# Kernel tuning notes

Hardware: AMD Instinct MI355X
Metric: run time of the kernel (lower is better)

Reference implementation:

```python
import jax, jax.numpy as jnp
import numpy as np

PI = float(np.pi)
LN_EPS = 1e-5
COS_EPS = 1e-6

D_HIDDEN, N_HEADS, D_HEAD, D_MLP = 1024, 16, 64, 4096
B, T = 4, 2048


def _xavier(key, shape):
    # torch xavier_uniform on 3D tensor: fan_in = shape[1]*shape[2]? torch uses
    # fan_in = shape[1] * receptive_field(shape[2:]), fan_out = shape[0] * rf.
    rf = 1
    for s in shape[2:]:
        rf *= s
    fan_in, fan_out = shape[1] * rf, shape[0] * rf
    bound = float(np.sqrt(6.0 / (fan_in + fan_out)))
    return jax.random.uniform(key, shape, jnp.float32, -bound, bound)


def setup_inputs() -> dict:
    key = jax.random.key(0)
    ks = jax.random.split(key, 10)
    x = jax.random.normal(ks[0], (B, T, D_HIDDEN), jnp.float32)
    W_Q = _xavier(ks[1], (N_HEADS, D_HIDDEN, 1))
    W_K = _xavier(ks[2], (N_HEADS, D_HIDDEN, 1))
    W_V = _xavier(ks[3], (N_HEADS, D_HIDDEN, D_HEAD))
    W_O = _xavier(ks[4], (D_HIDDEN, D_HEAD, N_HEADS))
    ln1_w = jnp.ones((D_HIDDEN,), jnp.float32)
    ln1_b = jnp.zeros((D_HIDDEN,), jnp.float32)
    ln2_w = jnp.ones((D_HIDDEN,), jnp.float32)
    ln2_b = jnp.zeros((D_HIDDEN,), jnp.float32)
    s1 = 1.0 / np.sqrt(D_HIDDEN)
    s2 = 1.0 / np.sqrt(D_MLP)
    W1 = jax.random.uniform(ks[5], (D_HIDDEN, D_MLP), jnp.float32, -s1, s1)
    b1 = jax.random.uniform(ks[6], (D_MLP,), jnp.float32, -s1, s1)
    W2 = jax.random.uniform(ks[7], (D_MLP, D_HIDDEN), jnp.float32, -s2, s2)
    b2 = jax.random.uniform(ks[8], (D_HIDDEN,), jnp.float32, -s2, s2)
    return {"x": x, "W_Q": W_Q, "W_K": W_K, "W_V": W_V, "W_O": W_O,
            "ln1_w": ln1_w, "ln1_b": ln1_b, "ln2_w": ln2_w, "ln2_b": ln2_b,
            "W1": W1, "b1": b1, "W2": W2, "b2": b2}


def _layer_norm(x, w, b):
    mu = jnp.mean(x, axis=-1, keepdims=True)
    var = jnp.mean(jnp.square(x - mu), axis=-1, keepdims=True)
    return (x - mu) * jax.lax.rsqrt(var + LN_EPS) * w + b


def _cos_attention(y, W_Q, W_K, W_V, W_O):
    q = jnp.einsum('btd,idh->btih', y, W_Q)  # (B,T,H,1)
    k = jnp.einsum('btd,idh->btih', y, W_K)  # (B,T,H,1)
    V = jnp.einsum('btd,idh->btih', y, W_V)  # (B,T,H,Dh)
    # use_tanh branch
    q = jnp.tanh(q) * (PI / 4)
    k = jnp.tanh(k) * (PI / 4)
    cos_k, sin_k = jnp.cos(k), jnp.sin(k)
    cos_KV = jnp.cumsum(cos_k * V, axis=1)
    sin_KV = jnp.cumsum(sin_k * V, axis=1)
    cos_Q, sin_Q = jnp.cos(q), jnp.sin(q)
    heads = cos_Q * cos_KV + sin_Q * sin_KV  # (B,T,H,Dh)
    # epsilon branch: normalizing denominator
    cos_K = jnp.cumsum(cos_k, axis=1)
    sin_K = jnp.cumsum(sin_k, axis=1)
    denom = cos_Q * cos_K + sin_Q * sin_K + COS_EPS  # (B,T,H,1)
    heads = heads / denom
    return jnp.einsum('dhi,btih->btd', W_O, heads)


def reference(x, W_Q, W_K, W_V, W_O, ln1_w, ln1_b, ln2_w, ln2_b, W1, b1, W2, b2):
    y = _layer_norm(x, ln1_w, ln1_b)
    x = x + _cos_attention(y, W_Q, W_K, W_V, W_O)
    y = _layer_norm(x, ln2_w, ln2_b)
    mlp = jnp.dot(jax.nn.gelu(jnp.dot(y, W1) + b1), W2) + b2
    return x + mlp
```

## Files before the change

### kernel.cpp

```cpp
#include <hip/hip_runtime.h>
#include <hip/hip_bf16.h>
#include <stdint.h>

typedef unsigned short u16;
typedef __attribute__((ext_vector_type(4))) unsigned int u32x4;
typedef __attribute__((ext_vector_type(8))) __bf16 bfx8;
typedef __attribute__((ext_vector_type(4))) float f32x4;

#define PI_F 3.14159265358979323846f

__device__ __forceinline__ float bf2f(u16 u) {
    unsigned v = ((unsigned)u) << 16; float f; __builtin_memcpy(&f, &v, 4); return f;
}
__device__ __forceinline__ u16 f2bf(float f) {
    unsigned u; __builtin_memcpy(&u, &f, 4);
    unsigned r = (u + 0x7fffu + ((u >> 16) & 1u)) >> 16; return (u16)r;
}

__device__ __forceinline__ void glds16(const u16* g, const u16* l) {
    __builtin_amdgcn_global_load_lds(
        (const __attribute__((address_space(1))) unsigned int*)(unsigned long long)g,
        (__attribute__((address_space(3))) unsigned int*)(unsigned int)(unsigned long long)l,
        16, 0, 0);
}

__global__ __launch_bounds__(256)
void tconv_kernel(const float* __restrict__ in, u16* __restrict__ out,
                  int R, int C, long inBatch, long outBatch)
{
    __shared__ float tile[64][65];
    const int tx = threadIdx.x & 63;
    const int ty = threadIdx.x >> 6;
    const int bc = blockIdx.x * 64;
    const int br = blockIdx.y * 64;
    const float* ip = in + (long)blockIdx.z * inBatch;
    u16* op = out + (long)blockIdx.z * outBatch;

    #pragma unroll
    for (int rr = ty; rr < 64; rr += 4) {
        int r = br + rr, c = bc + tx;
        tile[rr][tx] = (r < R && c < C) ? ip[(long)r * C + c] : 0.f;
    }
    __syncthreads();
    #pragma unroll
    for (int rr = ty; rr < 64; rr += 4) {
        int oc = bc + rr;
        int orr = br + tx;
        if (oc < C && orr < R)
            op[(long)oc * R + orr] = f2bf(tile[tx][rr]);
    }
}

template<bool DO_QK>
__global__ __launch_bounds__(256)
void ln_kernel(const float* __restrict__ X, const float* __restrict__ w,
               const float* __restrict__ b, u16* __restrict__ Ybf,
               const float* __restrict__ WQ, const float* __restrict__ WK,
               float* __restrict__ cqA, float* __restrict__ sqA,
               float* __restrict__ ckA, float* __restrict__ skA)
{
    __shared__ float yrow[1024];
    __shared__ float wsum[4], wsq[4];
    const int row = blockIdx.x;
    const int tid = threadIdx.x;
    const int lane = tid & 63;
    const int wv = tid >> 6;

    const float4 xv = ((const float4*)(X + (long)row * 1024))[tid];
    float s  = xv.x + xv.y + xv.z + xv.w;
    float sq = xv.x*xv.x + xv.y*xv.y + xv.z*xv.z + xv.w*xv.w;
    #pragma unroll
    for (int off = 32; off; off >>= 1) {
        s  += __shfl_down(s, off);
        sq += __shfl_down(sq, off);
    }
    if (lane == 0) { wsum[wv] = s; wsq[wv] = sq; }
    __syncthreads();
    const float ts = wsum[0] + wsum[1] + wsum[2] + wsum[3];
    const float tq = wsq[0] + wsq[1] + wsq[2] + wsq[3];
    const float mean = ts * (1.f / 1024.f);
    const float var  = tq * (1.f / 1024.f) - mean * mean;
    const float rstd = rsqrtf(var + 1e-5f);

    const float4 wv4 = ((const float4*)w)[tid];
    const float4 bv4 = ((const float4*)b)[tid];
    const float y0 = (xv.x - mean) * rstd * wv4.x + bv4.x;
    const float y1 = (xv.y - mean) * rstd * wv4.y + bv4.y;
    const float y2 = (xv.z - mean) * rstd * wv4.z + bv4.z;
    const float y3 = (xv.w - mean) * rstd * wv4.w + bv4.w;

    uint2 p;
    p.x = (unsigned)f2bf(y0) | ((unsigned)f2bf(y1) << 16);
    p.y = (unsigned)f2bf(y2) | ((unsigned)f2bf(y3) << 16);
    ((uint2*)(Ybf + (long)row * 1024))[tid] = p;

    if (DO_QK) {
        yrow[tid*4+0] = y0; yrow[tid*4+1] = y1;
        yrow[tid*4+2] = y2; yrow[tid*4+3] = y3;
        __syncthreads();
        #pragma unroll
        for (int i = 0; i < 4; ++i) {
            const int h = wv * 4 + i;
            const float* wqp = WQ + (long)h * 1024;
            const float* wkp = WK + (long)h * 1024;
            float dq = 0.f, dk = 0.f;
            #pragma unroll
            for (int j = 0; j < 16; ++j) {
                const float yv = yrow[lane + 64*j];
                dq = fmaf(yv, wqp[lane + 64*j], dq);
                dk = fmaf(yv, wkp[lane + 64*j], dk);
            }
            #pragma unroll
            for (int off = 32; off; off >>= 1) {
                dq += __shfl_down(dq, off);
                dk += __shfl_down(dk, off);
            }
            if (lane == 0) {
                const float aq = tanhf(dq) * (PI_F * 0.25f);
                const float ak = tanhf(dk) * (PI_F * 0.25f);
                float sv, cv;
                const long o = (long)h * 8192 + row;
                __sincosf(aq, &sv, &cv); cqA[o] = cv; sqA[o] = sv;
                __sincosf(ak, &sv, &cv); ckA[o] = cv; skA[o] = sv;
            }
        }
    }
}

__global__ __launch_bounds__(512)
void scan_kernel(const u16* __restrict__ V,
                 const float* __restrict__ cqA, const float* __restrict__ sqA,
                 const float* __restrict__ ckA, const float* __restrict__ skA,
                 u16* __restrict__ H)
{
    __shared__ float totcV[8][64], totsV[8][64];
    __shared__ float totc[8], tots[8];
    const int b = blockIdx.x >> 4;
    const int h = blockIdx.x & 15;
    const int wv = threadIdx.x >> 6;
    const int lane = threadIdx.x & 63;
    const long rowbase = (long)b * 2048;
    const long qbase = (long)h * 8192 + rowbase;
    const int t0 = wv * 256;

    const u16* vp = V + (rowbase + t0) * 1024 + (long)h * 64 + lane;

    float tc = 0.f, ts = 0.f, kc = 0.f, ks = 0.f;
    #pragma unroll 4
    for (int tt = 0; tt < 256; ++tt) {
        const float ck = ckA[qbase + t0 + tt];
        const float sk = skA[qbase + t0 + tt];
        const float vx = bf2f(vp[(long)tt * 1024]);
        tc = fmaf(ck, vx, tc); ts = fmaf(sk, vx, ts);
        kc += ck; ks += sk;
    }
    totcV[wv][lane] = tc; totsV[wv][lane] = ts;
    if (lane == 0) { totc[wv] = kc; tots[wv] = ks; }
    __syncthreads();

    float carC = 0.f, carS = 0.f, carKc = 0.f, carKs = 0.f;
    for (int w2 = 0; w2 < wv; ++w2) {
        carC += totcV[w2][lane]; carS += totsV[w2][lane];
        carKc += totc[w2]; carKs += tots[w2];
    }

    float csum = carC, ssum = carS, kcs = carKc, kss = carKs;
    u16* outp = H + (rowbase + t0) * 1024 + (long)h * 64 + lane;
    #pragma unroll 4
    for (int tt = 0; tt < 256; ++tt) {
        const long qo = qbase + t0 + tt;
        const float ck = ckA[qo], sk = skA[qo];
        const float cq = cqA[qo], sq2 = sqA[qo];
        const float vx = bf2f(vp[(long)tt * 1024]);
        csum = fmaf(ck, vx, csum); ssum = fmaf(sk, vx, ssum);
        kcs += ck; kss += sk;
        const float denom = cq * kcs + sq2 * kss + 1e-6f;
        const float hv = (cq * csum + sq2 * ssum) / denom;
        outp[(long)tt * 1024] = f2bf(hv);
    }
}

template<int EPI, int BN>
__global__ __launch_bounds__(512, 1)
void gemm6(const u16* __restrict__ A, const u16* __restrict__ B,
           void* __restrict__ Cout, const float* __restrict__ res,
           const float* __restrict__ bias, int N, int K, int nx)
{
    constexpr int NF = BN / 128;
    constexpr int WC = BN / 8;
    __shared__ u16 As[2 * 256 * 64];
    __shared__ u16 Bs[2 * BN * 64];

    const int tid  = threadIdx.x;
    const int lane = tid & 63;
    const int w    = tid >> 6;
    const int rr   = lane & 15;
    const int kq   = lane >> 4;

    const int L = blockIdx.x;
    const int xcd = L & 7;
    const int qq = L >> 3;
    const int brow = ((qq / nx) * 8 + xcd) * 256;
    const int bcol = (qq % nx) * BN;

    const int v = tid >> 3;
    const int chp = tid & 7;
    const int clog = (chp - (v & 7)) & 7;
    const u16* AgB = A + (long)(brow + v) * K + clog * 8;
    const u16* BgB = B + (long)(bcol + v) * K + clog * 8;

    const int ph0 = ((kq + (rr & 7)) & 7) * 16;
    const int ph1 = ((kq + 4 + (rr & 7)) & 7) * 16;
    const int arb = rr * 128;

    f32x4 acc[16][NF];
    #pragma unroll
    for (int i = 0; i < 16; ++i)
        #pragma unroll
        for (int j = 0; j < NF; ++j) acc[i][j] = (f32x4){0.f, 0.f, 0.f, 0.f};

    const int NT = K >> 6;

#define SA(nb, kn, s)  glds16(AgB + (kn) + (long)(s) * 64 * K, &As[(nb) * 16384 + (s) * 4096 + tid * 8])
#define SBG(nb, kn, s) glds16(BgB + (kn) + (long)(s) * 64 * K, &Bs[(nb) * (BN * 64) + (s) * 4096 + tid * 8])
#define BAR   asm volatile("s_barrier" ::: "memory")
#define LGKM0 asm volatile("s_waitcnt lgkmcnt(0)" ::: "memory")
#define VMC4  asm volatile("s_waitcnt vmcnt(4)" ::: "memory")
#define VMC2  asm volatile("s_waitcnt vmcnt(2)" ::: "memory")
#define SBR   __builtin_amdgcn_sched_barrier(0)

    if constexpr (BN == 256) { SBG(0,0,0); SBG(0,0,1); SBG(0,0,2); SBG(0,0,3); }
    else                     { SBG(0,0,0); SBG(0,0,1); }
    SA(0,0,0); SA(0,0,1); SA(0,0,2); SA(0,0,3);
    asm volatile("s_waitcnt vmcnt(0)" ::: "memory");
    BAR;

    for (int t = 0; t < NT; ++t) {
        const int cur = t & 1, nxt = cur ^ 1;
        const long kn = (long)((t + 1 < NT) ? (t + 1) : 0) * 64;
        const char* Ap = (const char*)As + cur * 32768;
        const char* Bp = (const char*)Bs + cur * (BN * 128);

        if constexpr (BN == 256) {
            bfx8 bF[4], aF[8];
            #pragma unroll
            for (int nf = 0; nf < 2; ++nf) {
                bF[nf*2+0] = *(const bfx8*)(Bp + w*4096 + nf*2048 + arb + ph0);
                bF[nf*2+1] = *(const bfx8*)(Bp + w*4096 + nf*2048 + arb + ph1);
            }
            #pragma unroll
            for (int mf = 0; mf < 4; ++mf) {
                aF[mf*2+0] = *(const bfx8*)(Ap + mf*2048 + arb + ph0);
                aF[mf*2+1] = *(const bfx8*)(Ap + mf*2048 + arb + ph1);
            }
            SBG(nxt, kn, 0); SBG(nxt, kn, 1);
            BAR; LGKM0; SBR;
            __builtin_amdgcn_s_setprio(1);
            #pragma unroll
            for (int mf = 0; mf < 4; ++mf)
                #pragma unroll
                for (int nf = 0; nf < 2; ++nf) {
                    acc[mf][nf] = __builtin_amdgcn_mfma_f32_16x16x32_bf16(aF[mf*2+0], bF[nf*2+0], acc[mf][nf], 0, 0, 0);
                    acc[mf][nf] = __builtin_amdgcn_mfma_f32_16x16x32_bf16(aF[mf*2+1], bF[nf*2+1], acc[mf][nf], 0, 0, 0);
                }
            __builtin_amdgcn_s_setprio(0); SBR; BAR;
            #pragma unroll
            for (int mf = 0; mf < 4; ++mf) {
                aF[mf*2+0] = *(const bfx8*)(Ap + 8192 + mf*2048 + arb + ph0);
                aF[mf*2+1] = *(const bfx8*)(Ap + 8192 + mf*2048 + arb + ph1);
            }
            SBG(nxt, kn, 2); SBG(nxt, kn, 3);
            BAR; LGKM0; SBR;
            __builtin_amdgcn_s_setprio(1);
            #pragma unroll
            for (int mf = 0; mf < 4; ++mf)
                #pragma unroll
                for (int nf = 0; nf < 2; ++nf) {
                    acc[4+mf][nf] = __builtin_amdgcn_mfma_f32_16x16x32_bf16(aF[mf*2+0], bF[nf*2+0], acc[4+mf][nf], 0, 0, 0);
                    acc[4+mf][nf] = __builtin_amdgcn_mfma_f32_16x16x32_bf16(aF[mf*2+1], bF[nf*2+1], acc[4+mf][nf], 0, 0, 0);
                }
            __builtin_amdgcn_s_setprio(0); SBR; VMC4; BAR;
            #pragma unroll
            for (int mf = 0; mf < 4; ++mf) {
                aF[mf*2+0] = *(const bfx8*)(Ap + 16384 + mf*2048 + arb + ph0);
                aF[mf*2+1] = *(const bfx8*)(Ap + 16384 + mf*2048 + arb + ph1);
            }
            SA(nxt, kn, 0); SA(nxt, kn, 1);
            BAR; LGKM0; SBR;
            __builtin_amdgcn_s_setprio(1);
            #pragma unroll
            for (int mf = 0; mf < 4; ++mf)
                #pragma unroll
                for (int nf = 0; nf < 2; ++nf) {
                    acc[8+mf][nf] = __builtin_amdgcn_mfma_f32_16x16x32_bf16(aF[mf*2+0], bF[nf*2+0], acc[8+mf][nf], 0, 0, 0);
                    acc[8+mf][nf] = __builtin_amdgcn_mfma_f32_16x16x32_bf16(aF[mf*2+1], bF[nf*2+1], acc[8+mf][nf], 0, 0, 0);
                }
            __builtin_amdgcn_s_setprio(0); SBR; BAR;
            #pragma unroll
            for (int mf = 0; mf < 4; ++mf) {
                aF[mf*2+0] = *(const bfx8*)(Ap + 24576 + mf*2048 + arb + ph0);
                aF[mf*2+1] = *(const bfx8*)(Ap + 24576 + mf*2048 + arb + ph1);
            }
            SA(nxt, kn, 2); SA(nxt, kn, 3);
            BAR; LGKM0; SBR;
            __builtin_amdgcn_s_setprio(1);
            #pragma unroll
            for (int mf = 0; mf < 4; ++mf)
                #pragma unroll
                for (int nf = 0; nf < 2; ++nf) {
                    acc[12+mf][nf] = __builtin_amdgcn_mfma_f32_16x16x32_bf16(aF[mf*2+0], bF[nf*2+0], acc[12+mf][nf], 0, 0, 0);
                    acc[12+mf][nf] = __builtin_amdgcn_mfma_f32_16x16x32_bf16(aF[mf*2+1], bF[nf*2+1], acc[12+mf][nf], 0, 0, 0);
                }
            __builtin_amdgcn_s_setprio(0); SBR; VMC2; BAR;
        } else {
            bfx8 bF[2], aF[16];
            bF[0] = *(const bfx8*)(Bp + w*2048 + arb + ph0);
            bF[1] = *(const bfx8*)(Bp + w*2048 + arb + ph1);
            #pragma unroll
            for (int mf = 0; mf < 8; ++mf) {
                aF[mf*2+0] = *(const bfx8*)(Ap + mf*2048 + arb + ph0);
                aF[mf*2+1] = *(const bfx8*)(Ap + mf*2048 + arb + ph1);
            }
            SBG(nxt, kn, 0); SBG(nxt, kn, 1); SA(nxt, kn, 0); SA(nxt, kn, 1);
            BAR; LGKM0; SBR;
            __builtin_amdgcn_s_setprio(1);
            #pragma unroll
            for (int mf = 0; mf < 8; ++mf) {
                acc[mf][0] = __builtin_amdgcn_mfma_f32_16x16x32_bf16(aF[mf*2+0], bF[0], acc[mf][0], 0, 0, 0);
                acc[mf][0] = __builtin_amdgcn_mfma_f32_16x16x32_bf16(aF[mf*2+1], bF[1], acc[mf][0], 0, 0, 0);
            }
            __builtin_amdgcn_s_setprio(0); SBR; VMC4; BAR;
            #pragma unroll
            for (int mf = 0; mf < 8; ++mf) {
                aF[mf*2+0] = *(const bfx8*)(Ap + 16384 + mf*2048 + arb + ph0);
                aF[mf*2+1] = *(const bfx8*)(Ap + 16384 + mf*2048 + arb + ph1);
            }
            SA(nxt, kn, 2); SA(nxt, kn, 3);
            BAR; LGKM0; SBR;
            __builtin_amdgcn_s_setprio(1);
            #pragma unroll
            for (int mf = 0; mf < 8; ++mf) {
                acc[8+mf][0] = __builtin_amdgcn_mfma_f32_16x16x32_bf16(aF[mf*2+0], bF[0], acc[8+mf][0], 0, 0, 0);
                acc[8+mf][0] = __builtin_amdgcn_mfma_f32_16x16x32_bf16(aF[mf*2+1], bF[1], acc[8+mf][0], 0, 0, 0);
            }
            __builtin_amdgcn_s_setprio(0); SBR; VMC2; BAR;
        }
    }
    asm volatile("s_waitcnt vmcnt(0)" ::: "memory");

#undef SA
#undef SBG
#undef BAR
#undef LGKM0
#undef VMC4
#undef VMC2
#undef SBR

    #pragma unroll
    for (int ai = 0; ai < 16; ++ai) {
        #pragma unroll
        for (int nf = 0; nf < NF; ++nf) {
            const int col = bcol + w * WC + nf * 16 + rr;
            #pragma unroll
            for (int r = 0; r < 4; ++r) {
                const int row = brow + ai * 16 + kq * 4 + r;
                const long idx = (long)row * N + col;
                const float vv = acc[ai][nf][r];
                if (EPI == 0) {
                    ((u16*)Cout)[idx] = f2bf(vv);
                } else if (EPI == 1) {
                    ((float*)Cout)[idx] = vv + res[idx];
                } else if (EPI == 2) {
                    const float hh = vv + bias[col];
                    const float z = 0.7978845608028654f * (hh + 0.044715f * hh * hh * hh);
                    const float e = __expf(2.f * z);
                    const float th = 1.f - 2.f / (e + 1.f);
                    ((u16*)Cout)[idx] = f2bf(0.5f * hh * (1.f + th));
                } else {
                    ((float*)Cout)[idx] = vv + res[idx] + bias[col];
                }
            }
        }
    }
}

extern "C" void kernel_launch(void* const* d_in, const int* in_sizes, int n_in,
                              void* d_out, int out_size, void* d_ws, size_t ws_size,
                              hipStream_t stream)
{
    (void)in_sizes; (void)n_in; (void)out_size; (void)ws_size;
    const float* x    = (const float*)d_in[0];
    const float* WQ   = (const float*)d_in[1];
    const float* WK   = (const float*)d_in[2];
    const float* WV   = (const float*)d_in[3];
    const float* WO   = (const float*)d_in[4];
    const float* ln1w = (const float*)d_in[5];
    const float* ln1b = (const float*)d_in[6];
    const float* ln2w = (const float*)d_in[7];
    const float* ln2b = (const float*)d_in[8];
    const float* W1   = (const float*)d_in[9];
    const float* b1   = (const float*)d_in[10];
    const float* W2   = (const float*)d_in[11];
    const float* b2   = (const float*)d_in[12];
    float* out = (float*)d_out;

    char* ws = (char*)d_ws;
    u16*   Ybf  = (u16*)(ws + 0);
    u16*   Vbf  = (u16*)(ws + 16777216);
    u16*   Hbf  = (u16*)(ws + 33554432);
    float* X2   = (float*)(ws + 50331648);
    u16*   H1   = (u16*)(ws + 83886080);
    u16*   WVT  = (u16*)(ws + 150994944);
    u16*   WOT  = (u16*)(ws + 153092096);
    u16*   W1T  = (u16*)(ws + 155189248);
    u16*   W2T  = (u16*)(ws + 163577856);
    float* CQ   = (float*)(ws + 171966464);
    float* SQ   = (float*)(ws + 172490752);
    float* CK   = (float*)(ws + 173015040);
    float* SK   = (float*)(ws + 173539328);

    tconv_kernel<<<dim3(1, 16, 16), 256, 0, stream>>>(WV, WVT, 1024, 64, 1024L*64, 64L*1024);
    tconv_kernel<<<dim3(1, 1, 1024), 256, 0, stream>>>(WO, WOT, 64, 16, 1024L, 1024L);
    tconv_kernel<<<dim3(64, 16, 1), 256, 0, stream>>>(W1, W1T, 1024, 4096, 0L, 0L);
    tconv_kernel<<<dim3(16, 64, 1), 256, 0, stream>>>(W2, W2T, 4096, 1024, 0L, 0L);

    ln_kernel<true><<<8192, 256, 0, stream>>>(x, ln1w, ln1b, Ybf, WQ, WK, CQ, SQ, CK, SK);

    gemm6<0, 128><<<256, 512, 0, stream>>>(Ybf, WVT, Vbf, nullptr, nullptr, 1024, 1024, 8);

    scan_kernel<<<64, 512, 0, stream>>>(Vbf, CQ, SQ, CK, SK, Hbf);

    gemm6<1, 128><<<256, 512, 0, stream>>>(Hbf, WOT, X2, x, nullptr, 1024, 1024, 8);

    ln_kernel<false><<<8192, 256, 0, stream>>>(X2, ln2w, ln2b, Ybf,
                                               nullptr, nullptr, nullptr, nullptr, nullptr, nullptr);

    gemm6<2, 256><<<512, 512, 0, stream>>>(Ybf, W1T, H1, nullptr, b1, 4096, 1024, 16);

    gemm6<3, 128><<<256, 512, 0, stream>>>(H1, W2T, out, X2, b2, 1024, 4096, 8);
}
```

Before: 510.9 us.

## Split cumulative scan into three-phase parallel scan and vectorize LN QK projection

Replaces the single 64-block scan kernel with a three-kernel decomposed scan: per-32-row chunk partial sums across 1024 blocks, a sequential carry pass over 64 chunks per batch-head, then a parallel finalize that emits the normalized heads. This raises parallelism far beyond 64 blocks on a many-CU GPU, at the cost of extra launches and a second read of V. The LN1 kernel also computes the Q/K projections with float4 loads over each thread's own elements plus a shared-memory cross-wave reduction, instead of staging the row in shared memory and doing strided scalar loads.

```diff
diff --git a/kernel.cpp b/kernel.cpp
--- a/kernel.cpp
+++ b/kernel.cpp
@@ -59,7 +59,6 @@
                float* __restrict__ cqA, float* __restrict__ sqA,
                float* __restrict__ ckA, float* __restrict__ skA)
 {
-    __shared__ float yrow[1024];
     __shared__ float wsum[4], wsq[4];
     const int row = blockIdx.x;
     const int tid = threadIdx.x;
@@ -94,89 +93,116 @@
     p.y = (unsigned)f2bf(y2) | ((unsigned)f2bf(y3) << 16);
     ((uint2*)(Ybf + (long)row * 1024))[tid] = p;
 
-    if (DO_QK) {
-        yrow[tid*4+0] = y0; yrow[tid*4+1] = y1;
-        yrow[tid*4+2] = y2; yrow[tid*4+3] = y3;
-        __syncthreads();
+    if constexpr (DO_QK) {
+        __shared__ float redq[16][4], redk[16][4];
         #pragma unroll
-        for (int i = 0; i < 4; ++i) {
-            const int h = wv * 4 + i;
-            const float* wqp = WQ + (long)h * 1024;
-            const float* wkp = WK + (long)h * 1024;
-            float dq = 0.f, dk = 0.f;
-            #pragma unroll
-            for (int j = 0; j < 16; ++j) {
-                const float yv = yrow[lane + 64*j];
-                dq = fmaf(yv, wqp[lane + 64*j], dq);
-                dk = fmaf(yv, wkp[lane + 64*j], dk);
-            }
+        for (int h = 0; h < 16; ++h) {
+            const float4 q4 = ((const float4*)WQ)[h * 256 + tid];
+            const float4 k4 = ((const float4*)WK)[h * 256 + tid];
+            float dq = y0*q4.x + y1*q4.y + y2*q4.z + y3*q4.w;
+            float dk = y0*k4.x + y1*k4.y + y2*k4.z + y3*k4.w;
             #pragma unroll
             for (int off = 32; off; off >>= 1) {
                 dq += __shfl_down(dq, off);
                 dk += __shfl_down(dk, off);
             }
-            if (lane == 0) {
-                const float aq = tanhf(dq) * (PI_F * 0.25f);
-                const float ak = tanhf(dk) * (PI_F * 0.25f);
-                float sv, cv;
-                const long o = (long)h * 8192 + row;
-                __sincosf(aq, &sv, &cv); cqA[o] = cv; sqA[o] = sv;
-                __sincosf(ak, &sv, &cv); ckA[o] = cv; skA[o] = sv;
-            }
+            if (lane == 0) { redq[h][wv] = dq; redk[h][wv] = dk; }
         }
-    }
-}
-
-__global__ __launch_bounds__(512)
-void scan_kernel(const u16* __restrict__ V,
-                 const float* __restrict__ cqA, const float* __restrict__ sqA,
-                 const float* __restrict__ ckA, const float* __restrict__ skA,
-                 u16* __restrict__ H)
-{
-    __shared__ float totcV[8][64], totsV[8][64];
-    __shared__ float totc[8], tots[8];
-    const int b = blockIdx.x >> 4;
-    const int h = blockIdx.x & 15;
-    const int wv = threadIdx.x >> 6;
-    const int lane = threadIdx.x & 63;
-    const long rowbase = (long)b * 2048;
-    const long qbase = (long)h * 8192 + rowbase;
-    const int t0 = wv * 256;
-
-    const u16* vp = V + (rowbase + t0) * 1024 + (long)h * 64 + lane;
+        __syncthreads();
+        if (tid < 32) {
+            const int h = tid >> 1;
+            const bool isk = tid & 1;
+            const float* rp = isk ? &redk[h][0] : &redq[h][0];
+            const float d = rp[0] + rp[1] + rp[2] + rp[3];
+            const float a = tanhf(d) * (PI_F * 0.25f);
+            float sv, cv; __sincosf(a, &sv, &cv);
+            const long o = (long)h * 8192 + row;
+            if (isk) { ckA[o] = cv; skA[o] = sv; }
+            else     { cqA[o] = cv; sqA[o] = sv; }
+        }
+    }
+}
+
+__global__ __launch_bounds__(256)
+void scanP(const u16* __restrict__ V, const float* __restrict__ ckA,
+           const float* __restrict__ skA,
+           float* __restrict__ PT, float* __restrict__ PS)
+{
+    const int bh = blockIdx.x >> 4;
+    const int macro = blockIdx.x & 15;
+    const int b = bh >> 4, h = bh & 15;
+    const int sub = threadIdx.x >> 6, c = threadIdx.x & 63;
+    const int g = macro * 4 + sub;
+    const int r0 = macro * 128 + sub * 32;
+    const long vbase = ((long)b * 2048 + r0) * 1024 + h * 64 + c;
+    const long qb = (long)h * 8192 + b * 2048 + r0;
 
     float tc = 0.f, ts = 0.f, kc = 0.f, ks = 0.f;
+    #pragma unroll 8
+    for (int i = 0; i < 32; ++i) {
+        const float ck = ckA[qb + i], sk = skA[qb + i];
+        const float v = bf2f(V[vbase + (long)i * 1024]);
+        tc = fmaf(ck, v, tc); ts = fmaf(sk, v, ts);
+        kc += ck; ks += sk;
+    }
+    float* pt = PT + (long)(bh * 64 + g) * 128;
+    pt[c] = tc; pt[64 + c] = ts;
+    if (c == 0) {
+        PS[(bh * 64 + g) * 2 + 0] = kc;
+        PS[(bh * 64 + g) * 2 + 1] = ks;
+    }
+}
+
+__global__ __launch_bounds__(64)
+void scanS(float* __restrict__ PT, float* __restrict__ PS)
+{
+    const int bh = blockIdx.x;
+    const int c = threadIdx.x;
+    float ac = 0.f, as = 0.f, akc = 0.f, aks = 0.f;
+    for (int g = 0; g < 64; ++g) {
+        float* pt = PT + (long)(bh * 64 + g) * 128;
+        const float pc = pt[c], ps = pt[64 + c];
+        pt[c] = ac; pt[64 + c] = as;
+        ac += pc; as += ps;
+        if (c == 0) {
+            float* pss = PS + (bh * 64 + g) * 2;
+            const float k0 = pss[0], k1 = pss[1];
+            pss[0] = akc; pss[1] = aks;
+            akc += k0; aks += k1;
+        }
+    }
+}
+
+__global__ __launch_bounds__(256)
+void scanE(const u16* __restrict__ V,
+           const float* __restrict__ cqA, const float* __restrict__ sqA,
+           const float* __restrict__ ckA, const float* __restrict__ skA,
+           const float* __restrict__ PT, const float* __restrict__ PS,
+           u16* __restrict__ H)
+{
+    const int bh = blockIdx.x >> 4;
+    const int macro = blockIdx.x & 15;
+    const int b = bh >> 4, h = bh & 15;
+    const int sub = threadIdx.x >> 6, c = threadIdx.x & 63;
+    const int g = macro * 4 + sub;
+    const int r0 = macro * 128 + sub * 32;
+    const long vbase = ((long)b * 2048 + r0) * 1024 + h * 64 + c;
+    const long qb = (long)h * 8192 + b * 2048 + r0;
+
+    const float* pt = PT + (long)(bh * 64 + g) * 128;
+    float csum = pt[c], ssum = pt[64 + c];
+    float kcs = PS[(bh * 64 + g) * 2 + 0];
+    float kss = PS[(bh * 64 + g) * 2 + 1];
+    u16* hp = H + vbase;
     #pragma unroll 4
-    for (int tt = 0; tt < 256; ++tt) {
-        const float ck = ckA[qbase + t0 + tt];
-        const float sk = skA[qbase + t0 + tt];
-        const float vx = bf2f(vp[(long)tt * 1024]);
-        tc = fmaf(ck, vx, tc); ts = fmaf(sk, vx, ts);
-        kc += ck; ks += sk;
-    }
-    totcV[wv][lane] = tc; totsV[wv][lane] = ts;
-    if (lane == 0) { totc[wv] = kc; tots[wv] = ks; }
-    __syncthreads();
-
-    float carC = 0.f, carS = 0.f, carKc = 0.f, carKs = 0.f;
-    for (int w2 = 0; w2 < wv; ++w2) {
-        carC += totcV[w2][lane]; carS += totsV[w2][lane];
-        carKc += totc[w2]; carKs += tots[w2];
-    }
-
-    float csum = carC, ssum = carS, kcs = carKc, kss = carKs;
-    u16* outp = H + (rowbase + t0) * 1024 + (long)h * 64 + lane;
-    #pragma unroll 4
-    for (int tt = 0; tt < 256; ++tt) {
-        const long qo = qbase + t0 + tt;
-        const float ck = ckA[qo], sk = skA[qo];
-        const float cq = cqA[qo], sq2 = sqA[qo];
-        const float vx = bf2f(vp[(long)tt * 1024]);
-        csum = fmaf(ck, vx, csum); ssum = fmaf(sk, vx, ssum);
+    for (int i = 0; i < 32; ++i) {
+        const float ck = ckA[qb + i], sk = skA[qb + i];
+        const float cq = cqA[qb + i], sq2 = sqA[qb + i];
+        const float v = bf2f(V[vbase + (long)i * 1024]);
+        csum = fmaf(ck, v, csum); ssum = fmaf(sk, v, ssum);
         kcs += ck; kss += sk;
         const float denom = cq * kcs + sq2 * kss + 1e-6f;
-        const float hv = (cq * csum + sq2 * ssum) / denom;
-        outp[(long)tt * 1024] = f2bf(hv);
+        hp[(long)i * 1024] = f2bf((cq * csum + sq2 * ssum) / denom);
     }
 }
 
@@ -418,6 +444,8 @@
     float* SQ   = (float*)(ws + 172490752);
     float* CK   = (float*)(ws + 173015040);
     float* SK   = (float*)(ws + 173539328);
+    float* PT   = (float*)(ws + 174063616);
+    float* PS   = (float*)(ws + 176160768);
 
     tconv_kernel<<<dim3(1, 16, 16), 256, 0, stream>>>(WV, WVT, 1024, 64, 1024L*64, 64L*1024);
     tconv_kernel<<<dim3(1, 1, 1024), 256, 0, stream>>>(WO, WOT, 64, 16, 1024L, 1024L);
@@ -428,7 +456,9 @@
 
     gemm6<0, 128><<<256, 512, 0, stream>>>(Ybf, WVT, Vbf, nullptr, nullptr, 1024, 1024, 8);
 
-    scan_kernel<<<64, 512, 0, stream>>>(Vbf, CQ, SQ, CK, SK, Hbf);
+    scanP<<<1024, 256, 0, stream>>>(Vbf, CK, SK, PT, PS);
+    scanS<<<64, 64, 0, stream>>>(PT, PS);
+    scanE<<<1024, 256, 0, stream>>>(Vbf, CQ, SQ, CK, SK, PT, PS, Hbf);
 
     gemm6<1, 128><<<256, 512, 0, stream>>>(Hbf, WOT, X2, x, nullptr, 1024, 1024, 8);
 
```

New measurement: 509.8 us. About the same (-0.2%).
